# Kernel optimization log

Measured on AMD Instinct MI355X. Metric: run time of the kernel, lower is better.

## Reference

```python
import jax, jax.numpy as jnp
import numpy as np

D_MODEL = 512
NUM_HEADS = 8
DEPTH = D_MODEL // NUM_HEADS
MAX_SEQ = 2048
B, L = 4, 1024


def setup_inputs() -> dict:
    key = jax.random.key(0)
    ks = jax.random.split(key, 13)
    s = 0.02
    return {
        "v": jax.random.normal(ks[0], (B, L, D_MODEL), jnp.float32),
        "k": jax.random.normal(ks[1], (B, L, D_MODEL), jnp.float32),
        "q": jax.random.normal(ks[2], (B, L, D_MODEL), jnp.float32),
        "mask": jnp.zeros((1, 1, L, L), jnp.float32),
        "wq_w": jax.random.normal(ks[3], (D_MODEL, D_MODEL), jnp.float32) * s,
        "wq_b": jnp.zeros((D_MODEL,), jnp.float32),
        "wk_w": jax.random.normal(ks[4], (D_MODEL, D_MODEL), jnp.float32) * s,
        "wk_b": jnp.zeros((D_MODEL,), jnp.float32),
        "wv_w": jax.random.normal(ks[5], (D_MODEL, D_MODEL), jnp.float32) * s,
        "wv_b": jnp.zeros((D_MODEL,), jnp.float32),
        "wo_w": jax.random.normal(ks[6], (D_MODEL, D_MODEL), jnp.float32) * s,
        "wo_b": jnp.zeros((D_MODEL,), jnp.float32),
        "pos_emb": jax.random.normal(ks[7], (MAX_SEQ, DEPTH), jnp.float32) * s,
    }


def _split_heads(x, batch):
    # [B, L, d_model] -> [B, H, L, depth]
    return x.reshape(batch, -1, NUM_HEADS, DEPTH).transpose(0, 2, 1, 3)


def reference(v, k, q, mask, wq_w, wq_b, wk_w, wk_b, wv_w, wv_b, wo_w, wo_b, pos_emb):
    batch, l_q, _ = q.shape
    qh = _split_heads(q @ wq_w + wq_b, batch)   # [B,H,Lq,depth]
    kh = _split_heads(k @ wk_w + wk_b, batch)   # [B,H,Lk,depth]
    vh = _split_heads(v @ wv_w + wv_b, batch)   # [B,H,Lk,depth]
    l_k = kh.shape[2]

    # relative position embedding slice: last l_q rows of pos_emb -> [Lq, depth]
    e = pos_emb[max(0, MAX_SEQ - l_q):, :]
    qe = jnp.einsum('nhld,md->nhlm', qh, e)     # [B,H,Lq,Lq]

    # upper-left triangular masking: keep entries with i + j >= Lq - 1
    keep = (jnp.arange(l_q)[:, None] + jnp.arange(l_q)[None, :]) >= (l_q - 1)
    qe = qe * keep.astype(qe.dtype)

    # skew trick: pad left on last dim, reshape [L, L+1]->[L+1, L], drop first row
    padded = jnp.pad(qe, ((0, 0), (0, 0), (0, 0), (1, 0)))
    srel = padded.reshape(batch, NUM_HEADS, l_q + 1, l_q)[:, :, 1:, :]  # [B,H,Lq,Lq]
    if l_k > l_q:
        srel = jnp.pad(srel, ((0, 0), (0, 0), (0, 0), (0, l_k - l_q)))
    elif l_k < l_q:
        srel = srel[..., :l_k]

    scale = 1.0 / jnp.sqrt(jnp.asarray(DEPTH, qh.dtype))
    logits = (jnp.einsum('nhld,nhmd->nhlm', qh, kh) + srel) * scale
    logits = logits + mask * (-1e9)
    attn = jax.nn.softmax(logits, axis=-1)      # [B,H,Lq,Lk]
    ctx = jnp.einsum('nhlm,nhmd->nhld', attn, vh)
    ctx = ctx.transpose(0, 2, 1, 3).reshape(batch, l_q, D_MODEL)
    out = ctx @ wo_w + wo_b
    return out, attn
```

## Files before the change

### kernel.cpp

```cpp
#include <hip/hip_runtime.h>

typedef __attribute__((ext_vector_type(4))) float f32x4;
typedef __attribute__((ext_vector_type(8))) short s16x8;
typedef __attribute__((ext_vector_type(4))) unsigned short u16x4;

__device__ inline unsigned short f2bf(float f) {
  unsigned int u = __builtin_bit_cast(unsigned int, f);
  u += 0x7fff + ((u >> 16) & 1);
  return (unsigned short)(u >> 16);
}
__device__ inline float bf2f(unsigned short u) {
  return __builtin_bit_cast(float, (unsigned int)u << 16);
}

__device__ __forceinline__ void async16(const void* g, void* s) {
  __builtin_amdgcn_global_load_lds(
      (const __attribute__((address_space(1))) unsigned int*)g,
      (__attribute__((address_space(3))) unsigned int*)s, 16, 0, 0);
}

__global__ __launch_bounds__(256) void cast_kernel(
    const float* __restrict__ v, const float* __restrict__ k, const float* __restrict__ q,
    const float* __restrict__ wq, const float* __restrict__ wk, const float* __restrict__ wv,
    const float* __restrict__ wo, const float* __restrict__ pos,
    unsigned short* __restrict__ qbf, unsigned short* __restrict__ kbf,
    unsigned short* __restrict__ vbf, unsigned short* __restrict__ wqT,
    unsigned short* __restrict__ wkT, unsigned short* __restrict__ wvT,
    unsigned short* __restrict__ woT, unsigned short* __restrict__ ebf) {
  int seg = blockIdx.y;
  int tid = blockIdx.x * blockDim.x + threadIdx.x;
  int stride = gridDim.x * blockDim.x;
  if (seg < 3) {
    const float* src = seg == 0 ? q : (seg == 1 ? k : v);
    unsigned short* dst = seg == 0 ? qbf : (seg == 1 ? kbf : vbf);
    for (int i = tid; i < 4096 * 512 / 4; i += stride) {
      f32x4 x = *(const f32x4*)&src[i * 4];
      u16x4 o = {f2bf(x[0]), f2bf(x[1]), f2bf(x[2]), f2bf(x[3])};
      *(u16x4*)&dst[i * 4] = o;
    }
  } else if (seg < 7) {
    const float* src = seg == 3 ? wq : seg == 4 ? wk : seg == 5 ? wv : wo;
    unsigned short* dst = seg == 3 ? wqT : seg == 4 ? wkT : seg == 5 ? wvT : woT;
    for (int i = tid; i < 512 * 128; i += stride) {
      int n = i >> 7, k0 = (i & 127) * 4;
      u16x4 o = {f2bf(src[(k0 + 0) * 512 + n]), f2bf(src[(k0 + 1) * 512 + n]),
                 f2bf(src[(k0 + 2) * 512 + n]), f2bf(src[(k0 + 3) * 512 + n])};
      *(u16x4*)&dst[n * 512 + k0] = o;
    }
  } else {
    for (int i = tid; i < 1024 * 64 / 4; i += stride) {
      f32x4 x = *(const f32x4*)&pos[1024 * 64 + i * 4];
      u16x4 o = {f2bf(x[0]), f2bf(x[1]), f2bf(x[2]), f2bf(x[3])};
      *(u16x4*)&ebf[i * 4] = o;
    }
  }
}

__device__ __forceinline__ void gemm_main(
    const unsigned short* __restrict__ A, const unsigned short* __restrict__ Bt,
    unsigned short* As, unsigned short* Bs, int r0, int c0, int tid,
    f32x4 acc[4][4]) {
  int lane = tid & 63, w = tid >> 6;
  int wr = w >> 1, wc = w & 1;
  int frow = lane & 15, kg = lane >> 4;
  for (int k0 = 0; k0 < 512; k0 += 32) {
#pragma unroll
    for (int j = 0; j < 2; ++j) {
      int t = tid + j * 256;
      int row = t >> 2, col = (t & 3) * 8;
      *(s16x8*)&As[row * 32 + col] = *(const s16x8*)&A[(size_t)(r0 + row) * 512 + k0 + col];
      *(s16x8*)&Bs[row * 32 + col] = *(const s16x8*)&Bt[(size_t)(c0 + row) * 512 + k0 + col];
    }
    __syncthreads();
    s16x8 af[4], bfr[4];
#pragma unroll
    for (int mi = 0; mi < 4; ++mi) af[mi] = *(s16x8*)&As[(wr * 64 + mi * 16 + frow) * 32 + kg * 8];
#pragma unroll
    for (int ni = 0; ni < 4; ++ni) bfr[ni] = *(s16x8*)&Bs[(wc * 64 + ni * 16 + frow) * 32 + kg * 8];
#pragma unroll
    for (int mi = 0; mi < 4; ++mi)
#pragma unroll
      for (int ni = 0; ni < 4; ++ni)
        acc[mi][ni] = __builtin_amdgcn_mfma_f32_16x16x32_bf16(af[mi], bfr[ni], acc[mi][ni], 0, 0, 0);
    __syncthreads();
  }
}

__global__ __launch_bounds__(256, 2) void proj3_kernel(
    const unsigned short* __restrict__ qbf, const unsigned short* __restrict__ kbf,
    const unsigned short* __restrict__ vbf, const unsigned short* __restrict__ wqT,
    const unsigned short* __restrict__ wkT, const unsigned short* __restrict__ wvT,
    const float* __restrict__ wq_b, const float* __restrict__ wk_b,
    const float* __restrict__ wv_b, unsigned short* __restrict__ qhw,
    unsigned short* __restrict__ khw, unsigned short* __restrict__ vhT) {
  __shared__ unsigned short As[128 * 32];
  __shared__ unsigned short Bs[128 * 32];
  int z = blockIdx.z;
  const unsigned short* A = z == 0 ? qbf : z == 1 ? kbf : vbf;
  const unsigned short* Bt = z == 0 ? wqT : z == 1 ? wkT : wvT;
  const float* bias = z == 0 ? wq_b : z == 1 ? wk_b : wv_b;
  unsigned short* outp = z == 0 ? qhw : z == 1 ? khw : vhT;
  int r0 = blockIdx.x * 128, c0 = blockIdx.y * 128;
  int tid = threadIdx.x;
  int lane = tid & 63, w = tid >> 6;
  int wr = w >> 1, wc = w & 1;
  int frow = lane & 15, kg = lane >> 4;
  f32x4 acc[4][4] = {};
  gemm_main(A, Bt, As, Bs, r0, c0, tid, acc);
#pragma unroll
  for (int ni = 0; ni < 4; ++ni) {
    int gc = c0 + wc * 64 + ni * 16 + frow;
    float bi = bias[gc];
#pragma unroll
    for (int mi = 0; mi < 4; ++mi) {
#pragma unroll
      for (int reg = 0; reg < 4; ++reg) {
        int gr = r0 + wr * 64 + mi * 16 + kg * 4 + reg;
        float val = acc[mi][ni][reg] + bi;
        if (z != 2) {
          outp[(size_t)((gr >> 10) * 8 + (gc >> 6)) * 65536 +
               (size_t)(gr & 1023) * 64 + (gc & 63)] = f2bf(val);
        } else {
          outp[(size_t)((gr >> 10) * 8 + (gc >> 6)) * 65536 +
               (size_t)(gc & 63) * 1024 + (gr & 1023)] = f2bf(val);
        }
      }
    }
  }
}

__global__ __launch_bounds__(256, 2) void gemm_out_kernel(
    const unsigned short* __restrict__ A, const unsigned short* __restrict__ Bt,
    const float* __restrict__ bias, float* __restrict__ outp) {
  __shared__ unsigned short As[128 * 32];
  __shared__ unsigned short Bs[128 * 32];
  int r0 = blockIdx.x * 128, c0 = blockIdx.y * 128;
  int tid = threadIdx.x;
  int lane = tid & 63, w = tid >> 6;
  int wr = w >> 1, wc = w & 1;
  int frow = lane & 15, kg = lane >> 4;
  f32x4 acc[4][4] = {};
  gemm_main(A, Bt, As, Bs, r0, c0, tid, acc);
#pragma unroll
  for (int ni = 0; ni < 4; ++ni) {
    int gc = c0 + wc * 64 + ni * 16 + frow;
    float bi = bias[gc];
#pragma unroll
    for (int mi = 0; mi < 4; ++mi)
#pragma unroll
      for (int reg = 0; reg < 4; ++reg) {
        int gr = r0 + wr * 64 + mi * 16 + kg * 4 + reg;
        outp[(size_t)gr * 512 + gc] = acc[mi][ni][reg] + bi;
      }
  }
}

__global__ __launch_bounds__(256, 2) void attn_kernel(
    const unsigned short* __restrict__ qh, const unsigned short* __restrict__ kh,
    const unsigned short* __restrict__ vhT, const unsigned short* __restrict__ ebf,
    const float* __restrict__ mask, float* __restrict__ attn_out,
    unsigned short* __restrict__ ctx) {
  __shared__ unsigned short S[16 * 1024];
  __shared__ unsigned short KV[2][8192];
  __shared__ float redmax[4][16], redsum[4][16];
  int nh = blockIdx.y;
  int l0 = blockIdx.x * 16;
  int tid = threadIdx.x;
  int lane = tid & 63, w = tid >> 6;
  int frow = lane & 15, kg = lane >> 4;

  auto sp = [&](int r, int c) -> unsigned short* {
    int byte = (r << 11) + (c << 1);
    byte ^= (r & 7) << 4;
    return (unsigned short*)((char*)S + byte);
  };

  auto stageKE = [&](const unsigned short* srcbase, int buf) {
#pragma unroll
    for (int i = 0; i < 4; ++i) {
      int u = (w * 4 + i) * 64 + lane;
      int row = u >> 3, pp = u & 7;
      async16(srcbase + (size_t)row * 64 + (size_t)((pp ^ (row & 7)) * 8),
              &KV[buf][(w * 4 + i) * 512]);
    }
  };
  auto stageV = [&](const unsigned short* srcbase, int c, int buf) {
#pragma unroll
    for (int i = 0; i < 4; ++i) {
      int u = (w * 4 + i) * 64 + lane;
      int row = u >> 4, pp = u & 15;
      int p = (pp & 8) | ((pp ^ (row & 7)) & 7);
      async16(srcbase + (size_t)row * 1024 + c * 128 + p * 8,
              &KV[buf][(w * 4 + i) * 512]);
    }
  };

  const unsigned short* qbase = qh + ((size_t)nh * 1024 + l0 + frow) * 64 + kg * 8;
  s16x8 qf0 = *(const s16x8*)(qbase);
  s16x8 qf1 = *(const s16x8*)(qbase + 32);

  int cmin = 1008 - l0;
  int cstart = cmin >> 7;
  stageKE(ebf + (size_t)cstart * 8192, cstart & 1);
  if (cstart + 1 < 8) stageKE(ebf + (size_t)(cstart + 1) * 8192, (cstart + 1) & 1);
  for (int c = cstart; c < 8; ++c) {
    int buf = c & 1;
    if (c + 1 < 8) { asm volatile("s_waitcnt vmcnt(4)" ::: "memory"); }
    else           { asm volatile("s_waitcnt vmcnt(0)" ::: "memory"); }
    __builtin_amdgcn_sched_barrier(0);
#pragma unroll
    for (int tt = 0; tt < 2; ++tt) {
      int j0 = c * 128 + (w * 2 + tt) * 16;
      if (j0 + 15 < cmin) continue;
      int lr = (w * 2 + tt) * 16 + frow;
      const char* base = (const char*)&KV[buf][0] + lr * 128;
      s16x8 b0 = *(const s16x8*)(base + ((kg ^ (lr & 7)) << 4));
      s16x8 b1 = *(const s16x8*)(base + (((4 + kg) ^ (lr & 7)) << 4));
      f32x4 a = {};
      a = __builtin_amdgcn_mfma_f32_16x16x32_bf16(b0, qf0, a, 0, 0, 0);
      a = __builtin_amdgcn_mfma_f32_16x16x32_bf16(b1, qf1, a, 0, 0, 0);
      u16x4 pk = {f2bf(a[0]), f2bf(a[1]), f2bf(a[2]), f2bf(a[3])};
      *(u16x4*)sp(frow, j0 + kg * 4) = pk;
    }
    asm volatile("s_waitcnt lgkmcnt(0)" ::: "memory");
    __builtin_amdgcn_sched_barrier(0);
    if (c + 2 < 8) stageKE(ebf + (size_t)(c + 2) * 8192, buf);
  }
  __syncthreads();

  f32x4 lg[16];
  const unsigned short* kbase = kh + (size_t)nh * 65536;
  stageKE(kbase, 0);
  stageKE(kbase + 8192, 1);
#pragma unroll
  for (int c = 0; c < 8; ++c) {
    int buf = c & 1;
    if (c + 1 < 8) { asm volatile("s_waitcnt vmcnt(4)" ::: "memory"); }
    else           { asm volatile("s_waitcnt vmcnt(0)" ::: "memory"); }
    __builtin_amdgcn_sched_barrier(0);
#pragma unroll
    for (int tt = 0; tt < 2; ++tt) {
      int lr = (w * 2 + tt) * 16 + frow;
      const char* base = (const char*)&KV[buf][0] + lr * 128;
      s16x8 b0 = *(const s16x8*)(base + ((kg ^ (lr & 7)) << 4));
      s16x8 b1 = *(const s16x8*)(base + (((4 + kg) ^ (lr & 7)) << 4));
      f32x4 a = {};
      a = __builtin_amdgcn_mfma_f32_16x16x32_bf16(b0, qf0, a, 0, 0, 0);
      a = __builtin_amdgcn_mfma_f32_16x16x32_bf16(b1, qf1, a, 0, 0, 0);
      lg[c * 2 + tt] = a;
    }
    asm volatile("s_waitcnt lgkmcnt(0)" ::: "memory");
    __builtin_amdgcn_sched_barrier(0);
    if (c + 2 < 8) stageKE(kbase + (size_t)(c + 2) * 8192, buf);
  }

  const unsigned short* vsrc = vhT + (size_t)nh * 65536;
  stageV(vsrc, 0, 0);
  stageV(vsrc, 1, 1);

  int lq = l0 + frow;
#pragma unroll
  for (int c = 0; c < 8; ++c) {
#pragma unroll
    for (int tt = 0; tt < 2; ++tt) {
      int t = c * 2 + tt;
      int m0k = c * 128 + (w * 2 + tt) * 16 + kg * 4;
      f32x4 mk = *(const f32x4*)&mask[(size_t)lq * 1024 + m0k];
#pragma unroll
      for (int reg = 0; reg < 4; ++reg) {
        int m = m0k + reg;
        float srel = (m <= lq) ? bf2f(*sp(frow, 1023 + m - lq)) : 0.f;
        lg[t][reg] = (lg[t][reg] + srel) * 0.125f + mk[reg] * -1e9f;
      }
    }
  }

  f32x4 vmax = lg[0];
#pragma unroll
  for (int t = 1; t < 16; ++t) {
#pragma unroll
    for (int reg = 0; reg < 4; ++reg) vmax[reg] = fmaxf(vmax[reg], lg[t][reg]);
  }
  float mx = fmaxf(fmaxf(vmax[0], vmax[1]), fmaxf(vmax[2], vmax[3]));
  mx = fmaxf(mx, __shfl_xor(mx, 16));
  mx = fmaxf(mx, __shfl_xor(mx, 32));
  float s = 0.f;
#pragma unroll
  for (int t = 0; t < 16; ++t) {
#pragma unroll
    for (int reg = 0; reg < 4; ++reg) {
      lg[t][reg] = __expf(lg[t][reg] - mx);
      s += lg[t][reg];
    }
  }
  s += __shfl_xor(s, 16);
  s += __shfl_xor(s, 32);
  if (lane < 16) {
    redmax[w][lane] = mx;
    redsum[w][lane] = s;
  }
  __syncthreads();

  float gmax = fmaxf(fmaxf(redmax[0][frow], redmax[1][frow]),
                     fmaxf(redmax[2][frow], redmax[3][frow]));
  float gsum = redsum[0][frow] * __expf(redmax[0][frow] - gmax) +
               redsum[1][frow] * __expf(redmax[1][frow] - gmax) +
               redsum[2][frow] * __expf(redmax[2][frow] - gmax) +
               redsum[3][frow] * __expf(redmax[3][frow] - gmax);
  float fac = __expf(mx - gmax) / gsum;

  size_t arow = ((size_t)nh * 1024 + lq) * 1024;
#pragma unroll
  for (int c = 0; c < 8; ++c) {
#pragma unroll
    for (int tt = 0; tt < 2; ++tt) {
      int t = c * 2 + tt;
      int m0k = c * 128 + (w * 2 + tt) * 16 + kg * 4;
      f32x4 pn;
#pragma unroll
      for (int reg = 0; reg < 4; ++reg) pn[reg] = lg[t][reg] * fac;
      *(f32x4*)&attn_out[arow + m0k] = pn;
      u16x4 pb = {f2bf(pn[0]), f2bf(pn[1]), f2bf(pn[2]), f2bf(pn[3])};
      *(u16x4*)sp(frow, m0k) = pb;
    }
  }
  __syncthreads();

  {
    f32x4 acc = {};
    int rd = w * 16 + frow;
#pragma unroll
    for (int c = 0; c < 8; ++c) {
      int buf = c & 1;
      if (c + 1 < 8) { asm volatile("s_waitcnt vmcnt(4)" ::: "memory"); }
      else           { asm volatile("s_waitcnt vmcnt(0)" ::: "memory"); }
      __builtin_amdgcn_sched_barrier(0);
#pragma unroll
      for (int ks = 0; ks < 4; ++ks) {
        s16x8 a = *(s16x8*)sp(frow, c * 128 + ks * 32 + kg * 8);
        int part = ks * 4 + kg;
        int partp = (part & 8) | ((part ^ (rd & 7)) & 7);
        s16x8 b = *(const s16x8*)((const char*)&KV[buf][0] + rd * 256 + partp * 16);
        acc = __builtin_amdgcn_mfma_f32_16x16x32_bf16(a, b, acc, 0, 0, 0);
      }
      asm volatile("s_waitcnt lgkmcnt(0)" ::: "memory");
      __builtin_amdgcn_sched_barrier(0);
      if (c + 2 < 8) stageV(vsrc, c + 2, buf);
    }
    int n = nh >> 3, h = nh & 7;
#pragma unroll
    for (int reg = 0; reg < 4; ++reg) {
      int rr = kg * 4 + reg;
      ctx[((size_t)(n * 1024 + l0 + rr)) * 512 + h * 64 + w * 16 + frow] = f2bf(acc[reg]);
    }
  }
}

extern "C" void kernel_launch(void* const* d_in, const int* in_sizes, int n_in,
                              void* d_out, int out_size, void* d_ws, size_t ws_size,
                              hipStream_t stream) {
  const float* v = (const float*)d_in[0];
  const float* k = (const float*)d_in[1];
  const float* q = (const float*)d_in[2];
  const float* mask = (const float*)d_in[3];
  const float* wq_w = (const float*)d_in[4];
  const float* wq_b = (const float*)d_in[5];
  const float* wk_w = (const float*)d_in[6];
  const float* wk_b = (const float*)d_in[7];
  const float* wv_w = (const float*)d_in[8];
  const float* wv_b = (const float*)d_in[9];
  const float* wo_w = (const float*)d_in[10];
  const float* wo_b = (const float*)d_in[11];
  const float* pos = (const float*)d_in[12];

  float* outp = (float*)d_out;
  float* attn_out = outp + (size_t)4 * 1024 * 512;

  char* ws = (char*)d_ws;
  unsigned short* qbf = (unsigned short*)(ws);
  unsigned short* kbf = (unsigned short*)(ws + ((size_t)4 << 20));
  unsigned short* vbf = (unsigned short*)(ws + ((size_t)8 << 20));
  unsigned short* wqT = (unsigned short*)(ws + ((size_t)12 << 20));
  unsigned short* wkT = (unsigned short*)(ws + ((size_t)12 << 20) + (512 << 10));
  unsigned short* wvT = (unsigned short*)(ws + ((size_t)13 << 20));
  unsigned short* woT = (unsigned short*)(ws + ((size_t)13 << 20) + (512 << 10));
  unsigned short* ebf = (unsigned short*)(ws + ((size_t)14 << 20));
  unsigned short* qhw = (unsigned short*)(ws + ((size_t)16 << 20));
  unsigned short* khw = (unsigned short*)(ws + ((size_t)20 << 20));
  unsigned short* vhT = (unsigned short*)(ws + ((size_t)24 << 20));
  unsigned short* ctx = qbf;

  cast_kernel<<<dim3(256, 8), 256, 0, stream>>>(v, k, q, wq_w, wk_w, wv_w, wo_w, pos,
                                                qbf, kbf, vbf, wqT, wkT, wvT, woT, ebf);
  proj3_kernel<<<dim3(32, 4, 3), 256, 0, stream>>>(qbf, kbf, vbf, wqT, wkT, wvT,
                                                   wq_b, wk_b, wv_b, qhw, khw, vhT);
  attn_kernel<<<dim3(64, 32), 256, 0, stream>>>(qhw, khw, vhT, ebf, mask, attn_out, ctx);
  gemm_out_kernel<<<dim3(32, 4), 256, 0, stream>>>(ctx, woT, wo_b, outp);
}
```

Before: 130.3 us.

## Double attention block to eight waves with split-K PV reduction

The attention kernel now runs 512 threads (8 waves) per block instead of 256. Each wave handles one 16-column tile per chunk for QE/QK and softmax, so it holds half as many logit registers. For the PV product the key dimension is split across two wave halves, and partial results are summed through a new shared-memory buffer before ctx is written. This raises the number of waves working on each block and lowers per-wave register pressure, at the cost of an extra barrier and the reduction step. The K prefetch is also issued before the barrier that follows the QE phase.

```diff
diff --git a/kernel.cpp b/kernel.cpp
--- a/kernel.cpp
+++ b/kernel.cpp
@@ -155,14 +155,15 @@
   }
 }
 
-__global__ __launch_bounds__(256, 2) void attn_kernel(
+__global__ __launch_bounds__(512, 2) void attn_kernel(
     const unsigned short* __restrict__ qh, const unsigned short* __restrict__ kh,
     const unsigned short* __restrict__ vhT, const unsigned short* __restrict__ ebf,
     const float* __restrict__ mask, float* __restrict__ attn_out,
     unsigned short* __restrict__ ctx) {
   __shared__ unsigned short S[16 * 1024];
   __shared__ unsigned short KV[2][8192];
-  __shared__ float redmax[4][16], redsum[4][16];
+  __shared__ float redmax[8][16], redsum[8][16];
+  __shared__ float ctxred[4][16][16];
   int nh = blockIdx.y;
   int l0 = blockIdx.x * 16;
   int tid = threadIdx.x;
@@ -177,21 +178,21 @@
 
   auto stageKE = [&](const unsigned short* srcbase, int buf) {
 #pragma unroll
-    for (int i = 0; i < 4; ++i) {
-      int u = (w * 4 + i) * 64 + lane;
-      int row = u >> 3, pp = u & 7;
-      async16(srcbase + (size_t)row * 64 + (size_t)((pp ^ (row & 7)) * 8),
-              &KV[buf][(w * 4 + i) * 512]);
+    for (int i = 0; i < 2; ++i) {
+      int u = i * 64 + lane;
+      int row = u >> 3, p = u & 7;
+      async16(srcbase + (size_t)(w * 16 + row) * 64 + ((p ^ (row & 7)) * 8),
+              &KV[buf][w * 1024 + i * 512]);
     }
   };
-  auto stageV = [&](const unsigned short* srcbase, int c, int buf) {
-#pragma unroll
-    for (int i = 0; i < 4; ++i) {
-      int u = (w * 4 + i) * 64 + lane;
-      int row = u >> 4, pp = u & 15;
-      int p = (pp & 8) | ((pp ^ (row & 7)) & 7);
-      async16(srcbase + (size_t)row * 1024 + c * 128 + p * 8,
-              &KV[buf][(w * 4 + i) * 512]);
+  auto stageV = [&](const unsigned short* vsrc, int c, int buf) {
+    int mh = w >> 2, dg = w & 3;
+#pragma unroll
+    for (int i = 0; i < 2; ++i) {
+      int u = i * 64 + lane;
+      int row = u >> 3, p = u & 7;
+      async16(vsrc + (size_t)(dg * 16 + row) * 1024 + mh * 512 + c * 64 + ((p ^ (row & 7)) * 8),
+              &KV[buf][w * 1024 + i * 512]);
     }
   };
 
@@ -205,17 +206,14 @@
   if (cstart + 1 < 8) stageKE(ebf + (size_t)(cstart + 1) * 8192, (cstart + 1) & 1);
   for (int c = cstart; c < 8; ++c) {
     int buf = c & 1;
-    if (c + 1 < 8) { asm volatile("s_waitcnt vmcnt(4)" ::: "memory"); }
+    if (c + 1 < 8) { asm volatile("s_waitcnt vmcnt(2)" ::: "memory"); }
     else           { asm volatile("s_waitcnt vmcnt(0)" ::: "memory"); }
     __builtin_amdgcn_sched_barrier(0);
-#pragma unroll
-    for (int tt = 0; tt < 2; ++tt) {
-      int j0 = c * 128 + (w * 2 + tt) * 16;
-      if (j0 + 15 < cmin) continue;
-      int lr = (w * 2 + tt) * 16 + frow;
-      const char* base = (const char*)&KV[buf][0] + lr * 128;
-      s16x8 b0 = *(const s16x8*)(base + ((kg ^ (lr & 7)) << 4));
-      s16x8 b1 = *(const s16x8*)(base + (((4 + kg) ^ (lr & 7)) << 4));
+    int j0 = c * 128 + w * 16;
+    if (j0 + 15 >= cmin) {
+      const char* base = (const char*)&KV[buf][0] + w * 2048 + frow * 128;
+      s16x8 b0 = *(const s16x8*)(base + ((kg ^ (frow & 7)) << 4));
+      s16x8 b1 = *(const s16x8*)(base + (((4 + kg) ^ (frow & 7)) << 4));
       f32x4 a = {};
       a = __builtin_amdgcn_mfma_f32_16x16x32_bf16(b0, qf0, a, 0, 0, 0);
       a = __builtin_amdgcn_mfma_f32_16x16x32_bf16(b1, qf1, a, 0, 0, 0);
@@ -226,29 +224,25 @@
     __builtin_amdgcn_sched_barrier(0);
     if (c + 2 < 8) stageKE(ebf + (size_t)(c + 2) * 8192, buf);
   }
-  __syncthreads();
-
-  f32x4 lg[16];
   const unsigned short* kbase = kh + (size_t)nh * 65536;
   stageKE(kbase, 0);
   stageKE(kbase + 8192, 1);
+  __syncthreads();
+
+  f32x4 lg[8];
 #pragma unroll
   for (int c = 0; c < 8; ++c) {
     int buf = c & 1;
-    if (c + 1 < 8) { asm volatile("s_waitcnt vmcnt(4)" ::: "memory"); }
+    if (c + 1 < 8) { asm volatile("s_waitcnt vmcnt(2)" ::: "memory"); }
     else           { asm volatile("s_waitcnt vmcnt(0)" ::: "memory"); }
     __builtin_amdgcn_sched_barrier(0);
-#pragma unroll
-    for (int tt = 0; tt < 2; ++tt) {
-      int lr = (w * 2 + tt) * 16 + frow;
-      const char* base = (const char*)&KV[buf][0] + lr * 128;
-      s16x8 b0 = *(const s16x8*)(base + ((kg ^ (lr & 7)) << 4));
-      s16x8 b1 = *(const s16x8*)(base + (((4 + kg) ^ (lr & 7)) << 4));
-      f32x4 a = {};
-      a = __builtin_amdgcn_mfma_f32_16x16x32_bf16(b0, qf0, a, 0, 0, 0);
-      a = __builtin_amdgcn_mfma_f32_16x16x32_bf16(b1, qf1, a, 0, 0, 0);
-      lg[c * 2 + tt] = a;
-    }
+    const char* base = (const char*)&KV[buf][0] + w * 2048 + frow * 128;
+    s16x8 b0 = *(const s16x8*)(base + ((kg ^ (frow & 7)) << 4));
+    s16x8 b1 = *(const s16x8*)(base + (((4 + kg) ^ (frow & 7)) << 4));
+    f32x4 a = {};
+    a = __builtin_amdgcn_mfma_f32_16x16x32_bf16(b0, qf0, a, 0, 0, 0);
+    a = __builtin_amdgcn_mfma_f32_16x16x32_bf16(b1, qf1, a, 0, 0, 0);
+    lg[c] = a;
     asm volatile("s_waitcnt lgkmcnt(0)" ::: "memory");
     __builtin_amdgcn_sched_barrier(0);
     if (c + 2 < 8) stageKE(kbase + (size_t)(c + 2) * 8192, buf);
@@ -261,36 +255,32 @@
   int lq = l0 + frow;
 #pragma unroll
   for (int c = 0; c < 8; ++c) {
-#pragma unroll
-    for (int tt = 0; tt < 2; ++tt) {
-      int t = c * 2 + tt;
-      int m0k = c * 128 + (w * 2 + tt) * 16 + kg * 4;
-      f32x4 mk = *(const f32x4*)&mask[(size_t)lq * 1024 + m0k];
-#pragma unroll
-      for (int reg = 0; reg < 4; ++reg) {
-        int m = m0k + reg;
-        float srel = (m <= lq) ? bf2f(*sp(frow, 1023 + m - lq)) : 0.f;
-        lg[t][reg] = (lg[t][reg] + srel) * 0.125f + mk[reg] * -1e9f;
-      }
+    int m0k = c * 128 + w * 16 + kg * 4;
+    f32x4 mk = *(const f32x4*)&mask[(size_t)lq * 1024 + m0k];
+#pragma unroll
+    for (int reg = 0; reg < 4; ++reg) {
+      int m = m0k + reg;
+      float srel = (m <= lq) ? bf2f(*sp(frow, 1023 + m - lq)) : 0.f;
+      lg[c][reg] = (lg[c][reg] + srel) * 0.125f + mk[reg] * -1e9f;
     }
   }
 
   f32x4 vmax = lg[0];
 #pragma unroll
-  for (int t = 1; t < 16; ++t) {
-#pragma unroll
-    for (int reg = 0; reg < 4; ++reg) vmax[reg] = fmaxf(vmax[reg], lg[t][reg]);
+  for (int c = 1; c < 8; ++c) {
+#pragma unroll
+    for (int reg = 0; reg < 4; ++reg) vmax[reg] = fmaxf(vmax[reg], lg[c][reg]);
   }
   float mx = fmaxf(fmaxf(vmax[0], vmax[1]), fmaxf(vmax[2], vmax[3]));
   mx = fmaxf(mx, __shfl_xor(mx, 16));
   mx = fmaxf(mx, __shfl_xor(mx, 32));
   float s = 0.f;
 #pragma unroll
-  for (int t = 0; t < 16; ++t) {
+  for (int c = 0; c < 8; ++c) {
 #pragma unroll
     for (int reg = 0; reg < 4; ++reg) {
-      lg[t][reg] = __expf(lg[t][reg] - mx);
-      s += lg[t][reg];
+      lg[c][reg] = __expf(lg[c][reg] - mx);
+      s += lg[c][reg];
     }
   }
   s += __shfl_xor(s, 16);
@@ -301,57 +291,60 @@
   }
   __syncthreads();
 
-  float gmax = fmaxf(fmaxf(redmax[0][frow], redmax[1][frow]),
-                     fmaxf(redmax[2][frow], redmax[3][frow]));
-  float gsum = redsum[0][frow] * __expf(redmax[0][frow] - gmax) +
-               redsum[1][frow] * __expf(redmax[1][frow] - gmax) +
-               redsum[2][frow] * __expf(redmax[2][frow] - gmax) +
-               redsum[3][frow] * __expf(redmax[3][frow] - gmax);
+  float gmax = redmax[0][frow];
+#pragma unroll
+  for (int wv = 1; wv < 8; ++wv) gmax = fmaxf(gmax, redmax[wv][frow]);
+  float gsum = 0.f;
+#pragma unroll
+  for (int wv = 0; wv < 8; ++wv) gsum += redsum[wv][frow] * __expf(redmax[wv][frow] - gmax);
   float fac = __expf(mx - gmax) / gsum;
 
   size_t arow = ((size_t)nh * 1024 + lq) * 1024;
 #pragma unroll
   for (int c = 0; c < 8; ++c) {
-#pragma unroll
-    for (int tt = 0; tt < 2; ++tt) {
-      int t = c * 2 + tt;
-      int m0k = c * 128 + (w * 2 + tt) * 16 + kg * 4;
-      f32x4 pn;
-#pragma unroll
-      for (int reg = 0; reg < 4; ++reg) pn[reg] = lg[t][reg] * fac;
-      *(f32x4*)&attn_out[arow + m0k] = pn;
-      u16x4 pb = {f2bf(pn[0]), f2bf(pn[1]), f2bf(pn[2]), f2bf(pn[3])};
-      *(u16x4*)sp(frow, m0k) = pb;
-    }
+    int m0k = c * 128 + w * 16 + kg * 4;
+    f32x4 pn;
+#pragma unroll
+    for (int reg = 0; reg < 4; ++reg) pn[reg] = lg[c][reg] * fac;
+    *(f32x4*)&attn_out[arow + m0k] = pn;
+    u16x4 pb = {f2bf(pn[0]), f2bf(pn[1]), f2bf(pn[2]), f2bf(pn[3])};
+    *(u16x4*)sp(frow, m0k) = pb;
   }
   __syncthreads();
 
   {
+    int mh = w >> 2, dg = w & 3;
     f32x4 acc = {};
-    int rd = w * 16 + frow;
 #pragma unroll
     for (int c = 0; c < 8; ++c) {
       int buf = c & 1;
-      if (c + 1 < 8) { asm volatile("s_waitcnt vmcnt(4)" ::: "memory"); }
+      if (c + 1 < 8) { asm volatile("s_waitcnt vmcnt(2)" ::: "memory"); }
       else           { asm volatile("s_waitcnt vmcnt(0)" ::: "memory"); }
       __builtin_amdgcn_sched_barrier(0);
-#pragma unroll
-      for (int ks = 0; ks < 4; ++ks) {
-        s16x8 a = *(s16x8*)sp(frow, c * 128 + ks * 32 + kg * 8);
-        int part = ks * 4 + kg;
-        int partp = (part & 8) | ((part ^ (rd & 7)) & 7);
-        s16x8 b = *(const s16x8*)((const char*)&KV[buf][0] + rd * 256 + partp * 16);
+      const char* vbase = (const char*)&KV[buf][0] + w * 2048 + frow * 128;
+#pragma unroll
+      for (int ks = 0; ks < 2; ++ks) {
+        s16x8 a = *(s16x8*)sp(frow, mh * 512 + c * 64 + ks * 32 + kg * 8);
+        s16x8 b = *(const s16x8*)(vbase + (((ks * 4 + kg) ^ (frow & 7)) << 4));
         acc = __builtin_amdgcn_mfma_f32_16x16x32_bf16(a, b, acc, 0, 0, 0);
       }
       asm volatile("s_waitcnt lgkmcnt(0)" ::: "memory");
       __builtin_amdgcn_sched_barrier(0);
       if (c + 2 < 8) stageV(vsrc, c + 2, buf);
     }
-    int n = nh >> 3, h = nh & 7;
-#pragma unroll
-    for (int reg = 0; reg < 4; ++reg) {
-      int rr = kg * 4 + reg;
-      ctx[((size_t)(n * 1024 + l0 + rr)) * 512 + h * 64 + w * 16 + frow] = f2bf(acc[reg]);
+    if (w >= 4) {
+#pragma unroll
+      for (int reg = 0; reg < 4; ++reg) ctxred[dg][kg * 4 + reg][frow] = acc[reg];
+    }
+    __syncthreads();
+    if (w < 4) {
+      int n = nh >> 3, h = nh & 7;
+#pragma unroll
+      for (int reg = 0; reg < 4; ++reg) {
+        float val = acc[reg] + ctxred[dg][kg * 4 + reg][frow];
+        ctx[((size_t)(n * 1024 + l0 + kg * 4 + reg)) * 512 + h * 64 + dg * 16 + frow] =
+            f2bf(val);
+      }
     }
   }
 }
@@ -394,6 +387,6 @@
                                                 qbf, kbf, vbf, wqT, wkT, wvT, woT, ebf);
   proj3_kernel<<<dim3(32, 4, 3), 256, 0, stream>>>(qbf, kbf, vbf, wqT, wkT, wvT,
                                                    wq_b, wk_b, wv_b, qhw, khw, vhT);
-  attn_kernel<<<dim3(64, 32), 256, 0, stream>>>(qhw, khw, vhT, ebf, mask, attn_out, ctx);
+  attn_kernel<<<dim3(64, 32), 512, 0, stream>>>(qhw, khw, vhT, ebf, mask, attn_out, ctx);
   gemm_out_kernel<<<dim3(32, 4), 256, 0, stream>>>(ctx, woT, wo_b, outp);
 }
```

Result: faster. 126.4 us (median of 2 runs) (-3.0%).
